# Kernel tuning notes

Measured on AMD Instinct MI355X. Metric: run time of the kernel, lower is better.

Reference implementation:

```python
import jax, jax.numpy as jnp
import numpy as np


def _bspline3_weights(t):
    # t in [0,1); cubic B-spline basis weights for taps at floor(x)-1..floor(x)+2
    t2 = t * t
    t3 = t2 * t
    w0 = (1.0 - 3.0 * t + 3.0 * t2 - t3) / 6.0   # (1-t)^3/6
    w1 = (4.0 - 6.0 * t2 + 3.0 * t3) / 6.0
    w2 = (1.0 + 3.0 * t + 3.0 * t2 - 3.0 * t3) / 6.0
    w3 = t3 / 6.0
    return jnp.stack([w0, w1, w2, w3], axis=-1)  # [..., 4]


def _grid_pull_cubic_circ(coeff, grid):
    # coeff: [X, Y, Z, C] spline coefficients; grid: [..., 3] coords in coeff voxels.
    # Cubic B-spline interpolation, circulant (wrap) boundary, extrapolate=True.
    X, Y, Z, C = coeff.shape
    f = jnp.floor(grid)
    t = grid - f                                  # fractional part, [..., 3]
    base = f.astype(jnp.int32) - 1                # leftmost tap, [..., 3]
    taps = jnp.arange(4, dtype=jnp.int32)
    ix = (base[..., 0, None] + taps) % X          # [..., 4]
    iy = (base[..., 1, None] + taps) % Y
    iz = (base[..., 2, None] + taps) % Z
    wx = _bspline3_weights(t[..., 0])             # [..., 4]
    wy = _bspline3_weights(t[..., 1])
    wz = _bspline3_weights(t[..., 2])
    out = jnp.zeros(grid.shape[:-1] + (C,), coeff.dtype)
    for a in range(4):
        wa, ia = wx[..., a], ix[..., a]
        for b in range(4):
            wab, ib = wa * wy[..., b], iy[..., b]
            for c in range(4):
                w = wab * wz[..., c]
                out = out + w[..., None] * coeff[ia, ib, iz[..., c]]
    return out


def _affine_grid(A, shape):
    # field[v] = A[:-1,:-1] @ v + A[:-1,-1], output [*shape, D]
    rngs = [jnp.arange(s, dtype=A.dtype) for s in shape]
    g = jnp.stack(jnp.meshgrid(*rngs, indexing='ij'), axis=-1)
    return g @ A[:-1, :-1].T + A[:-1, -1]


def setup_inputs() -> dict:
    key = jax.random.key(0)
    coeff = jax.random.normal(key, (80, 80, 80, 3), dtype=jnp.float32) * 2.0
    # well-conditioned voxel-to-world matrices
    affine = np.diag([2.0, 2.0, 2.0, 1.0]).astype(np.float32)          # field at 2mm
    fix_affine = np.eye(4, dtype=np.float32)                            # fixed at 1mm
    mov_affine = np.diag([1.5, 1.5, 1.5, 1.0]).astype(np.float32)
    mov_affine[:3, 3] = [5.0, 3.0, -2.0]
    return {
        'coeff': coeff,
        'affine': jnp.asarray(affine),
        'fix_affine': jnp.asarray(fix_affine),
        'mov_affine': jnp.asarray(mov_affine),
        'fd0': 160, 'fd1': 160, 'fd2': 160,
    }


def reference(coeff, affine, fix_affine, mov_affine, fd0, fd1, fd2):
    # SplineDisp.make_full
    fa = jnp.linalg.inv(affine) @ fix_affine      # fixed voxels -> field voxels
    ma = jnp.linalg.inv(mov_affine) @ affine      # field voxels -> moving voxels
    field = _affine_grid(fa, (fd0, fd1, fd2))     # [fd0, fd1, fd2, 3]
    field = field + _grid_pull_cubic_circ(coeff, field)
    field = field @ ma[:-1, :-1].T + ma[:-1, -1]
    return field
```

## Files before the change

kernel.cpp:

```cpp
#include <hip/hip_runtime.h>


#define CX 80
#define FD 160

__device__ inline void inv4(const float* m, float* inv) {
    inv[0]  =  m[5]*m[10]*m[15] - m[5]*m[11]*m[14] - m[9]*m[6]*m[15] + m[9]*m[7]*m[14] + m[13]*m[6]*m[11] - m[13]*m[7]*m[10];
    inv[4]  = -m[4]*m[10]*m[15] + m[4]*m[11]*m[14] + m[8]*m[6]*m[15] - m[8]*m[7]*m[14] - m[12]*m[6]*m[11] + m[12]*m[7]*m[10];
    inv[8]  =  m[4]*m[9]*m[15]  - m[4]*m[11]*m[13] - m[8]*m[5]*m[15] + m[8]*m[7]*m[13] + m[12]*m[5]*m[11] - m[12]*m[7]*m[9];
    inv[12] = -m[4]*m[9]*m[14]  + m[4]*m[10]*m[13] + m[8]*m[5]*m[14] - m[8]*m[6]*m[13] - m[12]*m[5]*m[10] + m[12]*m[6]*m[9];
    inv[1]  = -m[1]*m[10]*m[15] + m[1]*m[11]*m[14] + m[9]*m[2]*m[15] - m[9]*m[3]*m[14] - m[13]*m[2]*m[11] + m[13]*m[3]*m[10];
    inv[5]  =  m[0]*m[10]*m[15] - m[0]*m[11]*m[14] - m[8]*m[2]*m[15] + m[8]*m[3]*m[14] + m[12]*m[2]*m[11] - m[12]*m[3]*m[10];
    inv[9]  = -m[0]*m[9]*m[15]  + m[0]*m[11]*m[13] + m[8]*m[1]*m[15] - m[8]*m[3]*m[13] - m[12]*m[1]*m[11] + m[12]*m[3]*m[9];
    inv[13] =  m[0]*m[9]*m[14]  - m[0]*m[10]*m[13] - m[8]*m[1]*m[14] + m[8]*m[2]*m[13] + m[12]*m[1]*m[10] - m[12]*m[2]*m[9];
    inv[2]  =  m[1]*m[6]*m[15]  - m[1]*m[7]*m[14]  - m[5]*m[2]*m[15] + m[5]*m[3]*m[14] + m[13]*m[2]*m[7]  - m[13]*m[3]*m[6];
    inv[6]  = -m[0]*m[6]*m[15]  + m[0]*m[7]*m[14]  + m[4]*m[2]*m[15] - m[4]*m[3]*m[14] - m[12]*m[2]*m[7]  + m[12]*m[3]*m[6];
    inv[10] =  m[0]*m[5]*m[15]  - m[0]*m[7]*m[13]  - m[4]*m[1]*m[15] + m[4]*m[3]*m[13] + m[12]*m[1]*m[7]  - m[12]*m[3]*m[5];
    inv[14] = -m[0]*m[5]*m[14]  + m[0]*m[6]*m[13]  + m[4]*m[1]*m[14] - m[4]*m[2]*m[13] - m[12]*m[1]*m[6]  + m[12]*m[2]*m[5];
    inv[3]  = -m[1]*m[6]*m[11]  + m[1]*m[7]*m[10]  + m[5]*m[2]*m[11] - m[5]*m[3]*m[10] - m[9]*m[2]*m[7]   + m[9]*m[3]*m[6];
    inv[7]  =  m[0]*m[6]*m[11]  - m[0]*m[7]*m[10]  - m[4]*m[2]*m[11] + m[4]*m[3]*m[10] + m[8]*m[2]*m[7]   - m[8]*m[3]*m[6];
    inv[11] = -m[0]*m[5]*m[11]  + m[0]*m[7]*m[9]   + m[4]*m[1]*m[11] - m[4]*m[3]*m[9]  - m[8]*m[1]*m[7]   + m[8]*m[3]*m[5];
    inv[15] =  m[0]*m[5]*m[10]  - m[0]*m[6]*m[9]   - m[4]*m[1]*m[10] + m[4]*m[2]*m[9]  + m[8]*m[1]*m[6]   - m[8]*m[2]*m[5];
    float det = m[0]*inv[0] + m[1]*inv[4] + m[2]*inv[8] + m[3]*inv[12];
    float rdet = 1.0f / det;
    for (int i = 0; i < 16; ++i) inv[i] *= rdet;
}

__global__ void setup_mats(const float* __restrict__ affine,
                           const float* __restrict__ fix_aff,
                           const float* __restrict__ mov_aff,
                           float* __restrict__ M) {
    if (threadIdx.x != 0 || blockIdx.x != 0) return;
    float invA[16], invM[16];
    inv4(affine, invA);
    inv4(mov_aff, invM);
    for (int r = 0; r < 4; ++r)
        for (int c = 0; c < 4; ++c) {
            float s = 0.f;
            for (int k = 0; k < 4; ++k) s += invA[r*4+k] * fix_aff[k*4+c];
            M[r*4+c] = s;
        }
    for (int r = 0; r < 4; ++r)
        for (int c = 0; c < 4; ++c) {
            float s = 0.f;
            for (int k = 0; k < 4; ++k) s += invM[r*4+k] * affine[k*4+c];
            M[16 + r*4+c] = s;
        }
    float od = fabsf(M[1]) + fabsf(M[2]) + fabsf(M[4]) + fabsf(M[6]) + fabsf(M[8]) + fabsf(M[9]);
    int ok = (od < 1e-20f)
          && (M[0]  > 0.f) && (M[0]  <= 1.f)
          && (M[5]  > 0.f) && (M[5]  <= 1.f)
          && (M[10] > 0.f) && (M[10] <= 1.f);
    M[32] = ok ? 1.f : 0.f;
}

__device__ inline void bspline_w(float t, float w[4]) {
    float t2 = t * t;
    float t3 = t2 * t;
    const float s = 1.0f / 6.0f;
    w[0] = (1.f - 3.f*t + 3.f*t2 - t3) * s;
    w[1] = (4.f - 6.f*t2 + 3.f*t3) * s;
    w[2] = (1.f + 3.f*t + 3.f*t2 - 3.f*t3) * s;
    w[3] = t3 * s;
}

__device__ inline int wrap80(int v) {
    int r = v % CX;
    return (r < 0) ? r + CX : r;
}

__global__ __launch_bounds__(256) void pass_z(const float* __restrict__ coeff,
                                              const float* __restrict__ M,
                                              float4* __restrict__ T1) {
    if (M[32] == 0.f) return;
    int tid = blockIdx.x * 256 + threadIdx.x;
    int k = tid % FD;
    int r = tid / FD;
    float gz = M[10] * (float)k + M[11];
    float fz = floorf(gz);
    float wz[4];
    bspline_w(gz - fz, wz);
    int bz = wrap80((int)fz - 1);
    const float* base = coeff + r * (CX * 3);
    float a0 = 0.f, a1 = 0.f, a2 = 0.f;
#pragma unroll
    for (int c = 0; c < 4; ++c) {
        int zc = bz + c; if (zc >= CX) zc -= CX;
        const float* p = base + zc * 3;
        float w = wz[c];
        a0 = fmaf(w, p[0], a0);
        a1 = fmaf(w, p[1], a1);
        a2 = fmaf(w, p[2], a2);
    }
    float4 v; v.x = a0; v.y = a1; v.z = a2; v.w = 0.f;
    T1[tid] = v;
}

__global__ __launch_bounds__(256) void pass_y_c(const float* __restrict__ M,
                                                const float4* __restrict__ T1,
                                                float4* __restrict__ T2) {
    if (M[32] == 0.f) return;
    int tid = blockIdx.x * 256 + threadIdx.x;
    int k = tid % FD;
    int r = tid / FD;
    int jg = r % 20;
    int x = r / 20;
    int j0 = jg * 8;

    const float m5 = M[5], m7 = M[7];
    const float4* Tx = T1 + (size_t)x * CX * FD + k;

    float gy = m5 * (float)j0 + m7;
    float fy = floorf(gy);
    int nb = (int)fy - 1;
    float wy[4];
    bspline_w(gy - fy, wy);

    float4 w0, w1, w2, w3;
    {
        int y0 = wrap80(nb);
        int y1 = y0 + 1; if (y1 >= CX) y1 -= CX;
        int y2 = y1 + 1; if (y2 >= CX) y2 -= CX;
        int y3 = y2 + 1; if (y3 >= CX) y3 -= CX;
        w0 = Tx[(size_t)y0 * FD];
        w1 = Tx[(size_t)y1 * FD];
        w2 = Tx[(size_t)y2 * FD];
        w3 = Tx[(size_t)y3 * FD];
    }

    float4* To = T2 + ((size_t)(x * FD + j0)) * FD + k;
#pragma unroll
    for (int d = 0; d < 8; ++d) {
        if (d > 0) {
            int j = j0 + d;
            gy = m5 * (float)j + m7;
            fy = floorf(gy);
            int b2 = (int)fy - 1;
            if (b2 != nb) {
                w0 = w1; w1 = w2; w2 = w3;
                w3 = Tx[(size_t)wrap80(b2 + 3) * FD];
                nb = b2;
            }
            bspline_w(gy - fy, wy);
        }
        float a0 = wy[0]*w0.x + wy[1]*w1.x + wy[2]*w2.x + wy[3]*w3.x;
        float a1 = wy[0]*w0.y + wy[1]*w1.y + wy[2]*w2.y + wy[3]*w3.y;
        float a2 = wy[0]*w0.z + wy[1]*w1.z + wy[2]*w2.z + wy[3]*w3.z;
        float4 v; v.x = a0; v.y = a1; v.z = a2; v.w = 0.f;
        To[(size_t)d * FD] = v;
    }
}

__global__ __launch_bounds__(256) void pass_x_c(const float* __restrict__ coeff,
                                                const float* __restrict__ M,
                                                const float4* __restrict__ T2,
                                                float* __restrict__ out) {
    int tid = blockIdx.x * 256 + threadIdx.x;
    int k = tid % FD;
    int r = tid / FD;
    int j = r % FD;
    int ig = r / FD;
    int i0 = ig * 8;

    if (M[32] != 0.f) {
        const float m0 = M[0], m3 = M[3];
        const float gy = M[5] * (float)j + M[7];
        const float gz = M[10] * (float)k + M[11];
        const float4* Tjk = T2 + (size_t)j * FD + k;

        float gx = m0 * (float)i0 + m3;
        float fx = floorf(gx);
        int nb = (int)fx - 1;
        float wx[4];
        bspline_w(gx - fx, wx);

        float4 w0, w1, w2, w3;
        {
            int x0 = wrap80(nb);
            int x1 = x0 + 1; if (x1 >= CX) x1 -= CX;
            int x2 = x1 + 1; if (x2 >= CX) x2 -= CX;
            int x3 = x2 + 1; if (x3 >= CX) x3 -= CX;
            w0 = Tjk[(size_t)x0 * FD * FD];
            w1 = Tjk[(size_t)x1 * FD * FD];
            w2 = Tjk[(size_t)x2 * FD * FD];
            w3 = Tjk[(size_t)x3 * FD * FD];
        }

        float* po = out + (((size_t)(i0 * FD + j)) * FD + k) * 3;
#pragma unroll
        for (int d = 0; d < 8; ++d) {
            float gxd = gx;
            if (d > 0) {
                int i = i0 + d;
                gxd = m0 * (float)i + m3;
                float fx2 = floorf(gxd);
                int b2 = (int)fx2 - 1;
                if (b2 != nb) {
                    w0 = w1; w1 = w2; w2 = w3;
                    w3 = Tjk[(size_t)wrap80(b2 + 3) * FD * FD];
                    nb = b2;
                }
                bspline_w(gxd - fx2, wx);
            }
            float a0 = wx[0]*w0.x + wx[1]*w1.x + wx[2]*w2.x + wx[3]*w3.x;
            float a1 = wx[0]*w0.y + wx[1]*w1.y + wx[2]*w2.y + wx[3]*w3.y;
            float a2 = wx[0]*w0.z + wx[1]*w1.z + wx[2]*w2.z + wx[3]*w3.z;
            float ux = gxd + a0, uy = gy + a1, uz = gz + a2;
            po[0] = M[16]*ux + M[17]*uy + M[18]*uz + M[19];
            po[1] = M[20]*ux + M[21]*uy + M[22]*uz + M[23];
            po[2] = M[24]*ux + M[25]*uy + M[26]*uz + M[27];
            po += (size_t)FD * FD * 3;
        }
    } else {
        for (int d = 0; d < 8; ++d) {
            int i = i0 + d;
            float fi = (float)i, fj = (float)j, fk = (float)k;
            float gx = M[0]*fi + M[1]*fj + M[2]*fk  + M[3];
            float gy = M[4]*fi + M[5]*fj + M[6]*fk  + M[7];
            float gz = M[8]*fi + M[9]*fj + M[10]*fk + M[11];
            float fx = floorf(gx), fy = floorf(gy), fz = floorf(gz);
            float wx[4], wy[4], wz[4];
            bspline_w(gx - fx, wx);
            bspline_w(gy - fy, wy);
            bspline_w(gz - fz, wz);
            int bxw = wrap80((int)fx - 1);
            int byw = wrap80((int)fy - 1);
            int bzw = wrap80((int)fz - 1);
            int ox[4], oy[4], oz[4];
            for (int a = 0; a < 4; ++a) {
                int xa = bxw + a; if (xa >= CX) xa -= CX;
                int ya = byw + a; if (ya >= CX) ya -= CX;
                int za = bzw + a; if (za >= CX) za -= CX;
                ox[a] = xa * (CX*CX*3);
                oy[a] = ya * (CX*3);
                oz[a] = za * 3;
            }
            float a0 = 0.f, a1 = 0.f, a2 = 0.f;
            for (int a = 0; a < 4; ++a)
                for (int b = 0; b < 4; ++b)
                    for (int c = 0; c < 4; ++c) {
                        float w = wx[a] * wy[b] * wz[c];
                        const float* p = coeff + (ox[a] + oy[b] + oz[c]);
                        a0 = fmaf(w, p[0], a0);
                        a1 = fmaf(w, p[1], a1);
                        a2 = fmaf(w, p[2], a2);
                    }
            float ux = gx + a0, uy = gy + a1, uz = gz + a2;
            size_t o = ((size_t)(i * FD + j) * FD + k) * 3;
            out[o + 0] = M[16]*ux + M[17]*uy + M[18]*uz + M[19];
            out[o + 1] = M[20]*ux + M[21]*uy + M[22]*uz + M[23];
            out[o + 2] = M[24]*ux + M[25]*uy + M[26]*uz + M[27];
        }
    }
}

__global__ __launch_bounds__(256) void spline_direct(const float* __restrict__ coeff,
                                                     const float* __restrict__ M,
                                                     float* __restrict__ out) {
    int tid = blockIdx.x * 256 + threadIdx.x;
    int k = tid % FD;
    int r = tid / FD;
    int j = r % FD;
    int i = r / FD;
    float fi = (float)i, fj = (float)j, fk = (float)k;
    float gx = M[0]*fi + M[1]*fj + M[2]*fk  + M[3];
    float gy = M[4]*fi + M[5]*fj + M[6]*fk  + M[7];
    float gz = M[8]*fi + M[9]*fj + M[10]*fk + M[11];
    float fx = floorf(gx), fy = floorf(gy), fz = floorf(gz);
    float wx[4], wy[4], wz[4];
    bspline_w(gx - fx, wx);
    bspline_w(gy - fy, wy);
    bspline_w(gz - fz, wz);
    int bxw = wrap80((int)fx - 1);
    int byw = wrap80((int)fy - 1);
    int bzw = wrap80((int)fz - 1);
    int ox[4], oy[4], oz[4];
#pragma unroll
    for (int a = 0; a < 4; ++a) {
        int xa = bxw + a; if (xa >= CX) xa -= CX;
        int ya = byw + a; if (ya >= CX) ya -= CX;
        int za = bzw + a; if (za >= CX) za -= CX;
        ox[a] = xa * (CX*CX*3);
        oy[a] = ya * (CX*3);
        oz[a] = za * 3;
    }
    float a0 = 0.f, a1 = 0.f, a2 = 0.f;
#pragma unroll
    for (int a = 0; a < 4; ++a)
#pragma unroll
        for (int b = 0; b < 4; ++b)
#pragma unroll
            for (int c = 0; c < 4; ++c) {
                float w = wx[a] * wy[b] * wz[c];
                const float* p = coeff + (ox[a] + oy[b] + oz[c]);
                a0 = fmaf(w, p[0], a0);
                a1 = fmaf(w, p[1], a1);
                a2 = fmaf(w, p[2], a2);
            }
    float ux = gx + a0, uy = gy + a1, uz = gz + a2;
    float o0 = M[16]*ux + M[17]*uy + M[18]*uz + M[19];
    float o1 = M[20]*ux + M[21]*uy + M[22]*uz + M[23];
    float o2 = M[24]*ux + M[25]*uy + M[26]*uz + M[27];
    out[tid*3 + 0] = o0;
    out[tid*3 + 1] = o1;
    out[tid*3 + 2] = o2;
}

extern "C" void kernel_launch(void* const* d_in, const int* in_sizes, int n_in,
                              void* d_out, int out_size, void* d_ws, size_t ws_size,
                              hipStream_t stream) {
    const float* coeff   = (const float*)d_in[0];
    const float* affine  = (const float*)d_in[1];
    const float* fix_aff = (const float*)d_in[2];
    const float* mov_aff = (const float*)d_in[3];
    float* M   = (float*)d_ws;
    char*  ws  = (char*)d_ws;
    float4* T1 = (float4*)(ws + 256);
    float4* T2 = (float4*)(ws + 256 + (size_t)CX*CX*FD*16);
    float* out = (float*)d_out;

    const size_t need = 256 + (size_t)CX*CX*FD*16 + (size_t)CX*FD*FD*16;

    setup_mats<<<1, 64, 0, stream>>>(affine, fix_aff, mov_aff, M);

    if (ws_size >= need) {
        pass_z<<<(CX*CX*FD)/256, 256, 0, stream>>>(coeff, M, T1);
        pass_y_c<<<(CX*20*FD)/256, 256, 0, stream>>>(M, T1, T2);
        pass_x_c<<<(20*FD*FD)/256, 256, 0, stream>>>(coeff, M, T2, out);
    } else {
        spline_direct<<<(FD*FD*FD)/256, 256, 0, stream>>>(coeff, M, out);
    }
}
```

Before: 43.70 us.

## Fuse z and y spline passes into one kernel using shared memory

The separate z-pass and y-pass kernels are merged into one kernel. Each block loads NY coefficient rows for one x slice into LDS, computes the z-interpolated rows in shared memory, then applies the y interpolation and writes T2. This removes the global T1 intermediate (about 16 MB) and one launch. The cost is recomputing the z-pass for overlapping y rows across neighbouring blocks, and it assumes the y taps for 8 output rows fit within NY=12 source rows, which only holds for small y scale factors.

```diff
diff --git a/kernel.cpp b/kernel.cpp
--- a/kernel.cpp
+++ b/kernel.cpp
@@ -3,6 +3,7 @@
 
 #define CX 80
 #define FD 160
+#define NY 12
 
 __device__ inline void inv4(const float* m, float* inv) {
     inv[0]  =  m[5]*m[10]*m[15] - m[5]*m[11]*m[14] - m[9]*m[6]*m[15] + m[9]*m[7]*m[14] + m[13]*m[6]*m[11] - m[13]*m[7]*m[10];
@@ -69,85 +70,67 @@
     return (r < 0) ? r + CX : r;
 }
 
-__global__ __launch_bounds__(256) void pass_z(const float* __restrict__ coeff,
-                                              const float* __restrict__ M,
-                                              float4* __restrict__ T1) {
-    if (M[32] == 0.f) return;
-    int tid = blockIdx.x * 256 + threadIdx.x;
-    int k = tid % FD;
-    int r = tid / FD;
-    float gz = M[10] * (float)k + M[11];
-    float fz = floorf(gz);
-    float wz[4];
-    bspline_w(gz - fz, wz);
-    int bz = wrap80((int)fz - 1);
-    const float* base = coeff + r * (CX * 3);
-    float a0 = 0.f, a1 = 0.f, a2 = 0.f;
-#pragma unroll
-    for (int c = 0; c < 4; ++c) {
-        int zc = bz + c; if (zc >= CX) zc -= CX;
-        const float* p = base + zc * 3;
-        float w = wz[c];
-        a0 = fmaf(w, p[0], a0);
-        a1 = fmaf(w, p[1], a1);
-        a2 = fmaf(w, p[2], a2);
-    }
-    float4 v; v.x = a0; v.y = a1; v.z = a2; v.w = 0.f;
-    T1[tid] = v;
-}
-
-__global__ __launch_bounds__(256) void pass_y_c(const float* __restrict__ M,
-                                                const float4* __restrict__ T1,
+__global__ __launch_bounds__(256) void fused_zy(const float* __restrict__ coeff,
+                                                const float* __restrict__ M,
                                                 float4* __restrict__ T2) {
     if (M[32] == 0.f) return;
-    int tid = blockIdx.x * 256 + threadIdx.x;
-    int k = tid % FD;
-    int r = tid / FD;
-    int jg = r % 20;
-    int x = r / 20;
-    int j0 = jg * 8;
-
-    const float m5 = M[5], m7 = M[7];
-    const float4* Tx = T1 + (size_t)x * CX * FD + k;
-
-    float gy = m5 * (float)j0 + m7;
-    float fy = floorf(gy);
-    int nb = (int)fy - 1;
-    float wy[4];
-    bspline_w(gy - fy, wy);
-
-    float4 w0, w1, w2, w3;
-    {
-        int y0 = wrap80(nb);
-        int y1 = y0 + 1; if (y1 >= CX) y1 -= CX;
-        int y2 = y1 + 1; if (y2 >= CX) y2 -= CX;
-        int y3 = y2 + 1; if (y3 >= CX) y3 -= CX;
-        w0 = Tx[(size_t)y0 * FD];
-        w1 = Tx[(size_t)y1 * FD];
-        w2 = Tx[(size_t)y2 * FD];
-        w3 = Tx[(size_t)y3 * FD];
-    }
-
-    float4* To = T2 + ((size_t)(x * FD + j0)) * FD + k;
-#pragma unroll
-    for (int d = 0; d < 8; ++d) {
-        if (d > 0) {
-            int j = j0 + d;
-            gy = m5 * (float)j + m7;
-            fy = floorf(gy);
-            int b2 = (int)fy - 1;
-            if (b2 != nb) {
-                w0 = w1; w1 = w2; w2 = w3;
-                w3 = Tx[(size_t)wrap80(b2 + 3) * FD];
-                nb = b2;
-            }
-            bspline_w(gy - fy, wy);
-        }
-        float a0 = wy[0]*w0.x + wy[1]*w1.x + wy[2]*w2.x + wy[3]*w3.x;
-        float a1 = wy[0]*w0.y + wy[1]*w1.y + wy[2]*w2.y + wy[3]*w3.y;
-        float a2 = wy[0]*w0.z + wy[1]*w1.z + wy[2]*w2.z + wy[3]*w3.z;
-        float4 v; v.x = a0; v.y = a1; v.z = a2; v.w = 0.f;
-        To[(size_t)d * FD] = v;
+    __shared__ float  sc[NY * CX * 3];
+    __shared__ float4 st1[NY * FD];
+
+    int x  = blockIdx.x / 20;
+    int jt = blockIdx.x % 20;
+    int j0 = jt * 8;
+
+    const float m5 = M[5], m7 = M[7], m10 = M[10], m11 = M[11];
+    int by0 = (int)floorf(m5 * (float)j0 + m7) - 1;
+
+    const float* cx = coeff + (size_t)x * (CX * CX * 3);
+    for (int idx = threadIdx.x; idx < NY * CX * 3; idx += 256) {
+        int row = idx / (CX * 3);
+        int e   = idx % (CX * 3);
+        sc[idx] = cx[(size_t)wrap80(by0 + row) * (CX * 3) + e];
+    }
+    __syncthreads();
+
+    for (int item = threadIdx.x; item < NY * FD; item += 256) {
+        int yl = item / FD;
+        int k  = item % FD;
+        float gz = m10 * (float)k + m11;
+        float fz = floorf(gz);
+        float wz[4];
+        bspline_w(gz - fz, wz);
+        int bz = (int)fz - 1;
+        int z0 = wrap80(bz);
+        int z1 = z0 + 1; if (z1 >= CX) z1 -= CX;
+        int z2 = z1 + 1; if (z2 >= CX) z2 -= CX;
+        int z3 = z2 + 1; if (z3 >= CX) z3 -= CX;
+        const float* row = sc + yl * (CX * 3);
+        float4 v;
+        v.x = wz[0]*row[z0*3+0] + wz[1]*row[z1*3+0] + wz[2]*row[z2*3+0] + wz[3]*row[z3*3+0];
+        v.y = wz[0]*row[z0*3+1] + wz[1]*row[z1*3+1] + wz[2]*row[z2*3+1] + wz[3]*row[z3*3+1];
+        v.z = wz[0]*row[z0*3+2] + wz[1]*row[z1*3+2] + wz[2]*row[z2*3+2] + wz[3]*row[z3*3+2];
+        v.w = 0.f;
+        st1[item] = v;
+    }
+    __syncthreads();
+
+    for (int item = threadIdx.x; item < 8 * FD; item += 256) {
+        int jl = item / FD;
+        int k  = item % FD;
+        int j  = j0 + jl;
+        float gy = m5 * (float)j + m7;
+        float fy = floorf(gy);
+        float wy[4];
+        bspline_w(gy - fy, wy);
+        int row = ((int)fy - 1) - by0;
+        const float4* p = st1 + row * FD + k;
+        float4 w0 = p[0], w1 = p[FD], w2 = p[2*FD], w3 = p[3*FD];
+        float4 v;
+        v.x = wy[0]*w0.x + wy[1]*w1.x + wy[2]*w2.x + wy[3]*w3.x;
+        v.y = wy[0]*w0.y + wy[1]*w1.y + wy[2]*w2.y + wy[3]*w3.y;
+        v.z = wy[0]*w0.z + wy[1]*w1.z + wy[2]*w2.z + wy[3]*w3.z;
+        v.w = 0.f;
+        T2[((size_t)(x * FD + j)) * FD + k] = v;
     }
 }
 
@@ -298,12 +281,9 @@
                 a2 = fmaf(w, p[2], a2);
             }
     float ux = gx + a0, uy = gy + a1, uz = gz + a2;
-    float o0 = M[16]*ux + M[17]*uy + M[18]*uz + M[19];
-    float o1 = M[20]*ux + M[21]*uy + M[22]*uz + M[23];
-    float o2 = M[24]*ux + M[25]*uy + M[26]*uz + M[27];
-    out[tid*3 + 0] = o0;
-    out[tid*3 + 1] = o1;
-    out[tid*3 + 2] = o2;
+    out[tid*3 + 0] = M[16]*ux + M[17]*uy + M[18]*uz + M[19];
+    out[tid*3 + 1] = M[20]*ux + M[21]*uy + M[22]*uz + M[23];
+    out[tid*3 + 2] = M[24]*ux + M[25]*uy + M[26]*uz + M[27];
 }
 
 extern "C" void kernel_launch(void* const* d_in, const int* in_sizes, int n_in,
@@ -315,17 +295,15 @@
     const float* mov_aff = (const float*)d_in[3];
     float* M   = (float*)d_ws;
     char*  ws  = (char*)d_ws;
-    float4* T1 = (float4*)(ws + 256);
-    float4* T2 = (float4*)(ws + 256 + (size_t)CX*CX*FD*16);
+    float4* T2 = (float4*)(ws + 256);
     float* out = (float*)d_out;
 
-    const size_t need = 256 + (size_t)CX*CX*FD*16 + (size_t)CX*FD*FD*16;
+    const size_t need = 256 + (size_t)CX*FD*FD*16;
 
     setup_mats<<<1, 64, 0, stream>>>(affine, fix_aff, mov_aff, M);
 
     if (ws_size >= need) {
-        pass_z<<<(CX*CX*FD)/256, 256, 0, stream>>>(coeff, M, T1);
-        pass_y_c<<<(CX*20*FD)/256, 256, 0, stream>>>(M, T1, T2);
+        fused_zy<<<CX*20, 256, 0, stream>>>(coeff, M, T2);
         pass_x_c<<<(20*FD*FD)/256, 256, 0, stream>>>(coeff, M, T2, out);
     } else {
         spline_direct<<<(FD*FD*FD)/256, 256, 0, stream>>>(coeff, M, out);
```

New measurement: 51.69 us. 18.3% more time.
